# Kernel optimization log

Measured on AMD Instinct MI355X. Metric: run time of the kernel, lower is better.

The kernel has to match this reference:

```python
import jax, jax.numpy as jnp
import numpy as np

THRESHOLD = 0.1      # threshold_pos; threshold_neg = -THRESHOLD (encode uses +THRESHOLD on -diff)
TIME_STEPS = 16
BETA = 4.0           # surrogate_beta for fast_sigmoid
REFRACTORY = 2       # refractory_period
EPS = 1e-8

@jax.custom_vjp
def spike_fn(v):
    # forward: hard threshold spike (0/1)
    return (v >= THRESHOLD).astype(jnp.float32)

def _spike_fwd(v):
    return spike_fn(v), v

def _spike_bwd(v, g):
    # fast-sigmoid surrogate gradient centered at threshold
    s = jax.nn.sigmoid(BETA * (v - THRESHOLD))
    return (g * BETA * s * (1.0 - s),)

spike_fn.defvjp(_spike_fwd, _spike_bwd)

def setup_inputs() -> dict:
    key = jax.random.key(0)
    cpc_features = jax.random.normal(key, (8, 4096, 128), dtype=jnp.float32)
    return {"cpc_features": cpc_features}

def reference(cpc_features):
    # cpc_features: [B, S, F] -- temporal-contrast encode each feature channel along S
    diff = jnp.diff(cpc_features, axis=1, prepend=cpc_features[:, :1, :])   # [B,S,F]
    std = jnp.std(diff, axis=1, keepdims=True)                              # [B,1,F]
    nd = diff / (std + EPS)
    pos = spike_fn(nd)      # positive-contrast spikes, [B,S,F]
    neg = spike_fn(-nd)     # negative-contrast spikes, [B,S,F]
    # refractory pattern over time steps: t%3==0 -> pos, t%3==1 -> neg, else silent
    phase = (jnp.arange(TIME_STEPS) % (REFRACTORY + 1))[None, :, None, None]  # [1,T,1,1]
    spikes = jnp.where(phase == 0, pos[:, None, :, :],
                       jnp.where(phase == 1, neg[:, None, :, :], 0.0))
    return spikes  # [B, T, S, F]
```

## Files before the change

### kernel.cpp

```cpp
#include <hip/hip_runtime.h>
#include <math.h>

typedef float f32x4 __attribute__((ext_vector_type(4)));

constexpr int kB = 8;
constexpr int kS = 4096;
constexpr int kF = 128;
constexpr int kT = 16;
constexpr int kNCHUNK = 256;
constexpr int kSCHUNK = kS / kNCHUNK;

__global__ __launch_bounds__(128) void std_partial_kernel(
    const float* __restrict__ x, double* __restrict__ psum, double* __restrict__ psq) {
    const int b = blockIdx.x / kNCHUNK;
    const int c = blockIdx.x % kNCHUNK;
    const int f = threadIdx.x;
    const long base = ((long)(b * kS + c * kSCHUNK)) * kF + f;
    float prev = (c == 0) ? x[(long)b * kS * kF + f] : x[base - kF];
    double s1 = 0.0, s2 = 0.0;
    #pragma unroll
    for (int j = 0; j < kSCHUNK; ++j) {
        float cur = x[base + (long)j * kF];
        float d = cur - prev;
        s1 += (double)d;
        s2 += (double)d * (double)d;
        prev = cur;
    }
    const int o = c * (kB * kF) + b * kF + f;
    psum[o] = s1;
    psq[o]  = s2;
}

__global__ __launch_bounds__(64) void std_finish_kernel(
    const double* __restrict__ psum, const double* __restrict__ psq,
    float* __restrict__ denom) {
    const int i = blockIdx.x;
    const int lane = threadIdx.x;
    double s1 = 0.0, s2 = 0.0;
    #pragma unroll
    for (int j = 0; j < kNCHUNK / 64; ++j) {
        const long o = (long)(lane + j * 64) * (kB * kF) + i;
        s1 += psum[o];
        s2 += psq[o];
    }
    #pragma unroll
    for (int m = 32; m >= 1; m >>= 1) {
        s1 += __shfl_xor(s1, m, 64);
        s2 += __shfl_xor(s2, m, 64);
    }
    if (lane == 0) {
        const double mean = s1 / (double)kS;
        double var = s2 / (double)kS - mean * mean;
        if (var < 0.0) var = 0.0;
        const float stdf = (float)sqrt(var);
        denom[i] = stdf + 1e-8f;
    }
}

__global__ __launch_bounds__(128) void std_direct_kernel(
    const float* __restrict__ x, float* __restrict__ denom) {
    const int b = blockIdx.x;
    const int f = threadIdx.x;
    const long base = (long)b * kS * kF + f;
    float prev = x[base];
    double s1 = 0.0, s2 = 0.0;
    for (int s = 0; s < kS; ++s) {
        float cur = x[base + (long)s * kF];
        float d = cur - prev;
        s1 += (double)d;
        s2 += (double)d * (double)d;
        prev = cur;
    }
    const double mean = s1 / (double)kS;
    double var = s2 / (double)kS - mean * mean;
    if (var < 0.0) var = 0.0;
    denom[b * kF + f] = (float)sqrt(var) + 1e-8f;
}

__global__ __launch_bounds__(256) void spike_linear_kernel(
    const float* __restrict__ x, const float* __restrict__ denom,
    float* __restrict__ out) {
    const int i  = blockIdx.x * 256 + threadIdx.x;
    const int f4 = i & 31;
    const int s  = (i >> 5) & (kS - 1);
    const int t  = (i >> 17) & (kT - 1);
    const int b  = i >> 21;
    const int ph = t % 3;

    f32x4 v;
    v[0] = 0.0f; v[1] = 0.0f; v[2] = 0.0f; v[3] = 0.0f;
    if (ph != 2) {
        const long inoff = ((long)(b * kS + s)) * kF + f4 * 4;
        const f32x4 cur  = *(const f32x4*)(x + inoff);
        const f32x4 prev = (s == 0) ? cur : *(const f32x4*)(x + inoff - kF);
        const f32x4 dn   = *(const f32x4*)(denom + b * kF + f4 * 4);
        #pragma unroll
        for (int k = 0; k < 4; ++k) {
            const float nd = (cur[k] - prev[k]) / dn[k];
            const float sv = (ph == 0) ? nd : -nd;
            v[k] = (sv >= 0.1f) ? 1.0f : 0.0f;
        }
    }
    *(f32x4*)(out + ((long)i << 2)) = v;
}

extern "C" void kernel_launch(void* const* d_in, const int* in_sizes, int n_in,
                              void* d_out, int out_size, void* d_ws, size_t ws_size,
                              hipStream_t stream) {
    const float* x = (const float*)d_in[0];
    float* out = (float*)d_out;

    float* denom = (float*)d_ws;
    double* psum = (double*)((char*)d_ws + 4096);
    double* psq  = psum + (size_t)kNCHUNK * kB * kF;
    const size_t needed = 4096 + 2ull * kNCHUNK * kB * kF * sizeof(double);

    if (ws_size >= needed) {
        std_partial_kernel<<<kB * kNCHUNK, 128, 0, stream>>>(x, psum, psq);
        std_finish_kernel<<<kB * kF, 64, 0, stream>>>(psum, psq, denom);
    } else {
        std_direct_kernel<<<kB, 128, 0, stream>>>(x, denom);
    }

    const int n4 = kB * kT * kS * kF / 4;
    spike_linear_kernel<<<n4 / 256, 256, 0, stream>>>(x, denom, out);
}
```

Measured before the change: 274.7 us.

## Compute spikes once per element and split silent-slice zero fill

The per-output-element spike kernel is replaced by one that computes pos/neg spikes once per (b,s,f4) and writes them to all eleven active time slices. The five silent slices per batch are zeroed by a separate grid-stride fill kernel launched first. This removes redundant input loads and divides from recomputing each time step. The scattered strided stores across slices may reduce write coalescing, and one extra kernel launch is added.

```diff
diff --git a/kernel.cpp b/kernel.cpp
--- a/kernel.cpp
+++ b/kernel.cpp
@@ -77,31 +77,50 @@
     denom[b * kF + f] = (float)sqrt(var) + 1e-8f;
 }
 
-__global__ __launch_bounds__(256) void spike_linear_kernel(
+__global__ __launch_bounds__(256) void silent_fill_kernel(float* __restrict__ out) {
+    constexpr long kSliceQ = (long)kS * kF / 4;
+    constexpr long kTotal  = 40 * kSliceQ;
+    f32x4 z;
+    z[0] = 0.0f; z[1] = 0.0f; z[2] = 0.0f; z[3] = 0.0f;
+    f32x4* out4 = (f32x4*)out;
+    const long stride = (long)gridDim.x * 256;
+    for (long j = (long)blockIdx.x * 256 + threadIdx.x; j < kTotal; j += stride) {
+        const int  sl  = (int)(j >> 17);
+        const long pos = j & (kSliceQ - 1);
+        const int  b   = sl / 5;
+        const int  t   = 3 * (sl - b * 5) + 2;
+        out4[(((long)(b * kT + t)) << 17) + pos] = z;
+    }
+}
+
+__global__ __launch_bounds__(256) void spike_active_kernel(
     const float* __restrict__ x, const float* __restrict__ denom,
     float* __restrict__ out) {
-    const int i  = blockIdx.x * 256 + threadIdx.x;
-    const int f4 = i & 31;
-    const int s  = (i >> 5) & (kS - 1);
-    const int t  = (i >> 17) & (kT - 1);
-    const int b  = i >> 21;
-    const int ph = t % 3;
+    const int tid = threadIdx.x;
+    const int f4  = tid & 31;
+    const int row = tid >> 5;
+    const int b   = blockIdx.x >> 9;
+    const int s   = (blockIdx.x & 511) * 8 + row;
 
-    f32x4 v;
-    v[0] = 0.0f; v[1] = 0.0f; v[2] = 0.0f; v[3] = 0.0f;
-    if (ph != 2) {
-        const long inoff = ((long)(b * kS + s)) * kF + f4 * 4;
-        const f32x4 cur  = *(const f32x4*)(x + inoff);
-        const f32x4 prev = (s == 0) ? cur : *(const f32x4*)(x + inoff - kF);
-        const f32x4 dn   = *(const f32x4*)(denom + b * kF + f4 * 4);
-        #pragma unroll
-        for (int k = 0; k < 4; ++k) {
-            const float nd = (cur[k] - prev[k]) / dn[k];
-            const float sv = (ph == 0) ? nd : -nd;
-            v[k] = (sv >= 0.1f) ? 1.0f : 0.0f;
-        }
+    const long inoff = ((long)(b * kS + s)) * kF + f4 * 4;
+    const f32x4 cur  = *(const f32x4*)(x + inoff);
+    const f32x4 prev = (s == 0) ? cur : *(const f32x4*)(x + inoff - kF);
+    const f32x4 dn   = *(const f32x4*)(denom + b * kF + f4 * 4);
+
+    f32x4 pos, neg;
+    #pragma unroll
+    for (int k = 0; k < 4; ++k) {
+        const float nd = (cur[k] - prev[k]) / dn[k];
+        pos[k] = ( nd >= 0.1f) ? 1.0f : 0.0f;
+        neg[k] = (-nd >= 0.1f) ? 1.0f : 0.0f;
     }
-    *(f32x4*)(out + ((long)i << 2)) = v;
+
+    float* o = out + (((long)b * kT) * kS + s) * kF + f4 * 4;
+    const long ts = (long)kS * kF;
+    #pragma unroll
+    for (int t = 0; t < kT; t += 3) *(f32x4*)(o + (long)t * ts) = pos;
+    #pragma unroll
+    for (int t = 1; t < kT; t += 3) *(f32x4*)(o + (long)t * ts) = neg;
 }
 
 extern "C" void kernel_launch(void* const* d_in, const int* in_sizes, int n_in,
@@ -115,6 +134,8 @@
     double* psq  = psum + (size_t)kNCHUNK * kB * kF;
     const size_t needed = 4096 + 2ull * kNCHUNK * kB * kF * sizeof(double);
 
+    silent_fill_kernel<<<2048, 256, 0, stream>>>(out);
+
     if (ws_size >= needed) {
         std_partial_kernel<<<kB * kNCHUNK, 128, 0, stream>>>(x, psum, psq);
         std_finish_kernel<<<kB * kF, 64, 0, stream>>>(psum, psq, denom);
@@ -122,6 +143,5 @@
         std_direct_kernel<<<kB, 128, 0, stream>>>(x, denom);
     }
 
-    const int n4 = kB * kT * kS * kF / 4;
-    spike_linear_kernel<<<n4 / 256, 256, 0, stream>>>(x, denom, out);
+    spike_active_kernel<<<kB * (kS / 8), 256, 0, stream>>>(x, denom, out);
 }
```

Result: slower. 282.0 us (+2.6%).
